# Kernel tuning notes

Measured on AMD Instinct MI355X. Metric: run time of the kernel, lower is better.

The kernel has to match this reference:

```python
import jax, jax.numpy as jnp
import numpy as np

NB, B, C, L = 4, 16, 256, 4096
BN_EPS = 1e-5


def setup_inputs() -> dict:
    key = jax.random.key(0)
    ks = jax.random.split(key, 10)
    s = 0.02
    return {
        "x": jax.random.normal(ks[0], (NB, B, C, L), jnp.float32),
        "Wq": jax.random.normal(ks[1], (NB, C, C), jnp.float32) * s,
        "bq": jax.random.normal(ks[2], (NB, C), jnp.float32) * s,
        "Wk": jax.random.normal(ks[3], (NB, C, C), jnp.float32) * s,
        "bk": jax.random.normal(ks[4], (NB, C), jnp.float32) * s,
        "Wv": jax.random.normal(ks[5], (NB, C, C), jnp.float32) * s,
        "bv": jax.random.normal(ks[6], (NB, C), jnp.float32) * s,
        "Wo": jax.random.normal(ks[7], (NB, C, C), jnp.float32) * s,
        "bo": jax.random.normal(ks[8], (NB, C), jnp.float32) * s,
        "gamma": jnp.ones((NB, C), jnp.float32),
        "beta": jnp.zeros((NB, C), jnp.float32),
        "edge_w": jnp.ones((NB, NB), jnp.float32),
        "branch_imp": jnp.ones((NB,), jnp.float32),
    }


def _proj(W, b, x):
    # 1x1 Conv1d == per-branch channel mixing: [nb,o,c] x [nb,B,c,L] -> [nb,B,o,L]
    return jnp.einsum('noc,nbcl->nbol', W, x) + b[:, None, :, None]


def reference(x, Wq, bq, Wk, bk, Wv, bv, Wo, bo, gamma, beta, edge_w, branch_imp):
    feat_dim = x.shape[2]
    scale = jnp.sqrt(jnp.asarray(feat_dim, x.dtype))
    q = _proj(Wq, bq, x)
    k = _proj(Wk, bk, x)
    v = _proj(Wv, bv, x)
    # descriptors: [nb, B, C, 2] = (mean over L, max over L)
    qd = jnp.stack([q.mean(axis=-1), q.max(axis=-1)], axis=-1)
    kd = jnp.stack([k.mean(axis=-1), k.max(axis=-1)], axis=-1)
    # mean over 2x2 bmm entries == (sum_p qd)(sum_q kd) summed over C, / 4
    scores = jnp.einsum('ibcp,jbcq->ijb', qd, kd) / (4.0 * scale)
    scores = scores * edge_w[:, :, None]
    attn = jax.nn.softmax(scores, axis=1) * jax.nn.softmax(branch_imp)[None, :, None]
    # weighted aggregation over source branches j
    agg = jnp.einsum('ijb,jbcl->ibcl', attn, v)
    out = _proj(Wo, bo, agg)
    # BatchNorm1d (training-mode batch statistics over B and L per channel, per branch)
    mean = out.mean(axis=(1, 3), keepdims=True)
    var = out.var(axis=(1, 3), keepdims=True)
    bn = (out - mean) * jax.lax.rsqrt(var + BN_EPS)
    bn = bn * gamma[:, None, :, None] + beta[:, None, :, None]
    return jax.nn.relu(bn) + x
```

## Files before the change

### kernel.cpp

```cpp
#include <hip/hip_runtime.h>
#include <stdint.h>
#include <stddef.h>

#define NBR 4
#define BSZ 16
#define CHN 256
#define LEN 4096
#define NB_B 64
#define BL   65536
#define BN_EPS 1e-5f
#define W_EL (NBR*CHN*CHN)

typedef unsigned short ushortT;
typedef unsigned short ushort4_t __attribute__((ext_vector_type(4)));
typedef unsigned short ushort8_t __attribute__((ext_vector_type(8)));
typedef short bf16x8 __attribute__((ext_vector_type(8)));
typedef float f32x4 __attribute__((ext_vector_type(4)));

__device__ __forceinline__ float bf2f(ushortT u) {
    return __uint_as_float(((unsigned)u) << 16);
}
__device__ __forceinline__ ushortT f2bf(float f) {
    unsigned b = __float_as_uint(f);
    return (ushortT)((b + 0x7FFFu + ((b >> 16) & 1u)) >> 16);
}
__device__ __forceinline__ unsigned encf(float f) {
    unsigned b = __float_as_uint(f);
    return (b & 0x80000000u) ? ~b : (b | 0x80000000u);
}
__device__ __forceinline__ float decf(unsigned u) {
    unsigned b = (u & 0x80000000u) ? (u ^ 0x80000000u) : ~u;
    return __uint_as_float(b);
}

__device__ __forceinline__ int swzX(int row, int cb) {
    return row * 512 + (cb ^ ((row & 7) << 4) ^ (((row >> 3) & 3) << 7));
}
__device__ __forceinline__ int swzW(int row, int cb) {
    return row * 128 + (cb ^ ((row & 7) << 4));
}

template <bool BF16IN>
__device__ __forceinline__ void stage_x(const void* act, ushortT* sX, int z, int lbase, int tid)
{
    const int ls = tid & 127;
    const int gh = tid >> 7;
    if (BF16IN) {
        const ushortT* xp = (const ushortT*)act + (size_t)z * CHN * LEN + lbase + ls;
#pragma unroll
        for (int g = 0; g < 16; ++g) {
            int c0 = (gh * 16 + g) * 8;
            ushort8_t u;
#pragma unroll
            for (int i = 0; i < 8; ++i) u[i] = xp[(size_t)(c0 + i) * LEN];
            *(ushort8_t*)((char*)sX + swzX(ls, c0 * 2)) = u;
        }
    } else {
        const float* xp = (const float*)act + (size_t)z * CHN * LEN + lbase + ls;
#pragma unroll
        for (int g = 0; g < 16; ++g) {
            int c0 = (gh * 16 + g) * 8;
            ushort8_t u;
#pragma unroll
            for (int i = 0; i < 8; ++i) u[i] = f2bf(xp[(size_t)(c0 + i) * LEN]);
            *(ushort8_t*)((char*)sX + swzX(ls, c0 * 2)) = u;
        }
    }
}

__device__ __forceinline__ void stage_w_load(const ushortT* Wb, int obase, int kb, int tid,
                                             ushort8_t wreg[4])
{
    const int r = tid >> 1;
    const int h = tid & 1;
    const ushortT* wp = Wb + (size_t)(obase + r) * CHN + kb + h * 32;
#pragma unroll
    for (int i = 0; i < 4; ++i) wreg[i] = *(const ushort8_t*)(wp + i * 8);
}
__device__ __forceinline__ void stage_w_write(ushortT* sW, int tid, const ushort8_t wreg[4])
{
    const int r = tid >> 1;
    const int h = tid & 1;
#pragma unroll
    for (int i = 0; i < 4; ++i)
        *(ushort8_t*)((char*)sW + swzW(r, h * 64 + i * 16)) = wreg[i];
}

__device__ __forceinline__ void mfma_chunk(const ushortT* sX, const ushortT* sW,
                                           f32x4 acc[4][4], int wr, int wc, int lane, int kb)
{
    const int am = wr * 64 + (lane & 15);
    const int bo = wc * 64 + (lane & 15);
    const int kg = (lane >> 4) * 16;
#pragma unroll
    for (int s = 0; s < 2; ++s) {
        bf16x8 a[4], b[4];
#pragma unroll
        for (int mf = 0; mf < 4; ++mf)
            a[mf] = *(const bf16x8*)((const char*)sX + swzX(am + mf * 16, kb * 2 + s * 64 + kg));
#pragma unroll
        for (int nf = 0; nf < 4; ++nf)
            b[nf] = *(const bf16x8*)((const char*)sW + swzW(bo + nf * 16, s * 64 + kg));
#pragma unroll
        for (int mf = 0; mf < 4; ++mf)
#pragma unroll
            for (int nf = 0; nf < 4; ++nf)
                acc[mf][nf] = __builtin_amdgcn_mfma_f32_16x16x32_bf16(a[mf], b[nf], acc[mf][nf], 0, 0, 0);
    }
}

__global__ __launch_bounds__(256, 2)
void qkv_kernel(const float* __restrict__ x, const ushortT* __restrict__ Wbf,
                const float* __restrict__ bv,
                float* __restrict__ qsum, unsigned* __restrict__ qmax,
                float* __restrict__ ksum, unsigned* __restrict__ kmax,
                ushortT* __restrict__ vbuf)
{
    __shared__ ushortT sX[128 * 256];
    __shared__ ushortT sW[128 * 64];
    const int tid = threadIdx.x;
    const int lane = tid & 63;
    const int wv = tid >> 6;
    const int wr = wv >> 1, wc = wv & 1;
    const int lbase = blockIdx.x * 128;
    const int z = blockIdx.y;
    const int n = z >> 4;

    stage_x<false>(x, sX, z, lbase, tid);

    ushort8_t wreg[4];
    stage_w_load(Wbf + (size_t)n * CHN * CHN, 0, 0, tid, wreg);

    for (int w = 0; w < 3; ++w) {
        for (int ot = 0; ot < 2; ++ot) {
            const int obase = ot * 128;
            f32x4 acc[4][4];
            const f32x4 z4 = {0.f, 0.f, 0.f, 0.f};
#pragma unroll
            for (int mf = 0; mf < 4; ++mf)
#pragma unroll
                for (int nf = 0; nf < 4; ++nf) acc[mf][nf] = z4;

#pragma unroll
            for (int kb = 0; kb < 4; ++kb) {
                __syncthreads();
                stage_w_write(sW, tid, wreg);
                int cidx = (w * 2 + ot) * 4 + kb + 1;
                if (cidx < 24) {
                    int nw = cidx >> 3, not_ = (cidx >> 2) & 1, nkb = cidx & 3;
                    stage_w_load(Wbf + ((size_t)nw * NBR + n) * CHN * CHN,
                                 not_ * 128, nkb * 64, tid, wreg);
                }
                __syncthreads();
                mfma_chunk(sX, sW, acc, wr, wc, lane, kb * 64);
            }

            if (w < 2) {
                float* rs = (w == 0) ? qsum : ksum;
                unsigned* rm = (w == 0) ? qmax : kmax;
#pragma unroll
                for (int nf = 0; nf < 4; ++nf) {
                    float s = 0.f, m = -3.4e38f;
#pragma unroll
                    for (int mf = 0; mf < 4; ++mf)
#pragma unroll
                        for (int r = 0; r < 4; ++r) {
                            float v = acc[mf][nf][r];
                            s += v; m = fmaxf(m, v);
                        }
                    s += __shfl_xor(s, 16); s += __shfl_xor(s, 32);
                    m = fmaxf(m, __shfl_xor(m, 16)); m = fmaxf(m, __shfl_xor(m, 32));
                    if (lane < 16) {
                        int o = obase + wc * 64 + nf * 16 + lane;
                        atomicAdd(&rs[z * CHN + o], s);
                        atomicMax(&rm[z * CHN + o], encf(m));
                    }
                }
            } else {
#pragma unroll
                for (int nf = 0; nf < 4; ++nf) {
                    int o = obase + wc * 64 + nf * 16 + (lane & 15);
                    float bvv = bv[n * CHN + o];
#pragma unroll
                    for (int mf = 0; mf < 4; ++mf) {
                        int l = lbase + wr * 64 + mf * 16 + ((lane >> 4) << 2);
                        ushort4_t u;
#pragma unroll
                        for (int r = 0; r < 4; ++r) u[r] = f2bf(acc[mf][nf][r] + bvv);
                        *(ushort4_t*)(vbuf + (size_t)(z * CHN + o) * LEN + l) = u;
                    }
                }
            }
        }
    }
}

__global__ __launch_bounds__(256, 2)
void ogemm_kernel(const ushortT* __restrict__ agg, const ushortT* __restrict__ Wbo,
                  const float* __restrict__ bo_,
                  float* __restrict__ bnsum, float* __restrict__ bnss,
                  ushortT* __restrict__ outpre)
{
    __shared__ ushortT sX[128 * 256];
    __shared__ ushortT sW[128 * 64];
    const int tid = threadIdx.x;
    const int lane = tid & 63;
    const int wv = tid >> 6;
    const int wr = wv >> 1, wc = wv & 1;
    const int lbase = blockIdx.x * 128;
    const int z = blockIdx.y;
    const int n = z >> 4;
    const ushortT* Wb = Wbo + (size_t)n * CHN * CHN;

    stage_x<true>(agg, sX, z, lbase, tid);

    ushort8_t wreg[4];
    stage_w_load(Wb, 0, 0, tid, wreg);

    for (int ot = 0; ot < 2; ++ot) {
        const int obase = ot * 128;
        f32x4 acc[4][4];
        const f32x4 z4 = {0.f, 0.f, 0.f, 0.f};
#pragma unroll
        for (int mf = 0; mf < 4; ++mf)
#pragma unroll
            for (int nf = 0; nf < 4; ++nf) acc[mf][nf] = z4;

#pragma unroll
        for (int kb = 0; kb < 4; ++kb) {
            __syncthreads();
            stage_w_write(sW, tid, wreg);
            int cidx = ot * 4 + kb + 1;
            if (cidx < 8) {
                int not_ = (cidx >> 2) & 1, nkb = cidx & 3;
                stage_w_load(Wb, not_ * 128, nkb * 64, tid, wreg);
            }
            __syncthreads();
            mfma_chunk(sX, sW, acc, wr, wc, lane, kb * 64);
        }

#pragma unroll
        for (int nf = 0; nf < 4; ++nf) {
            int o = obase + wc * 64 + nf * 16 + (lane & 15);
            float bb = bo_[n * CHN + o];
            float s = 0.f, q2 = 0.f;
#pragma unroll
            for (int mf = 0; mf < 4; ++mf) {
                int l = lbase + wr * 64 + mf * 16 + ((lane >> 4) << 2);
                ushort4_t u;
#pragma unroll
                for (int r = 0; r < 4; ++r) {
                    float v = acc[mf][nf][r] + bb;
                    u[r] = f2bf(v);
                    s += v; q2 += v * v;
                }
                *(ushort4_t*)(outpre + (size_t)(z * CHN + o) * LEN + l) = u;
            }
            s += __shfl_xor(s, 16); s += __shfl_xor(s, 32);
            q2 += __shfl_xor(q2, 16); q2 += __shfl_xor(q2, 32);
            if (lane < 16) {
                atomicAdd(&bnsum[n * CHN + o], s);
                atomicAdd(&bnss[n * CHN + o], q2);
            }
        }
    }
}

__global__ void wcvt_kernel(const float* __restrict__ Wq, const float* __restrict__ Wk,
                            const float* __restrict__ Wv, const float* __restrict__ Wo,
                            ushortT* __restrict__ Wbf)
{
    int t = blockIdx.x * 256 + threadIdx.x;
    const int per = W_EL / 4;
    if (t < 4 * per) {
        const float* srcs[4] = {Wq, Wk, Wv, Wo};
        int w = t / per;
        int r = t - w * per;
        float4 f = *(const float4*)(srcs[w] + (size_t)r * 4);
        ushort4_t u = {f2bf(f.x), f2bf(f.y), f2bf(f.z), f2bf(f.w)};
        *(ushort4_t*)(Wbf + (size_t)w * W_EL + (size_t)r * 4) = u;
    }
}

__global__ void attn_kernel(const float* __restrict__ qsum, const unsigned* __restrict__ qmax,
                            const float* __restrict__ ksum, const unsigned* __restrict__ kmax,
                            const float* __restrict__ bq, const float* __restrict__ bk,
                            const float* __restrict__ edge, const float* __restrict__ bimp,
                            float* __restrict__ attn)
{
    __shared__ float sc[NBR][NBR][BSZ];
    int tid = threadIdx.x;
    int i = tid >> 6, j = (tid >> 4) & 3, b = tid & 15;
    float s = 0.f;
    const float invL = 1.0f / (float)LEN;
    for (int c = 0; c < CHN; ++c) {
        int qi = (i * BSZ + b) * CHN + c;
        int ki = (j * BSZ + b) * CHN + c;
        float sq = qsum[qi] * invL + decf(qmax[qi]) + 2.f * bq[i * CHN + c];
        float sk = ksum[ki] * invL + decf(kmax[ki]) + 2.f * bk[j * CHN + c];
        s += sq * sk;
    }
    sc[i][j][b] = s * edge[i * 4 + j] * (1.0f / 64.0f);
    __syncthreads();
    if (tid < 64) {
        int ii = tid >> 4, bb = tid & 15;
        float m = -3.4e38f;
        for (int jj = 0; jj < 4; ++jj) m = fmaxf(m, sc[ii][jj][bb]);
        float e[4]; float sum = 0.f;
        for (int jj = 0; jj < 4; ++jj) { e[jj] = __expf(sc[ii][jj][bb] - m); sum += e[jj]; }
        float bm = fmaxf(fmaxf(bimp[0], bimp[1]), fmaxf(bimp[2], bimp[3]));
        float be[4]; float bs = 0.f;
        for (int jj = 0; jj < 4; ++jj) { be[jj] = __expf(bimp[jj] - bm); bs += be[jj]; }
        for (int jj = 0; jj < 4; ++jj)
            attn[(ii * 4 + jj) * BSZ + bb] = (e[jj] / sum) * (be[jj] / bs);
    }
}

__global__ __launch_bounds__(256)
void agg_kernel(const ushortT* __restrict__ v, const float* __restrict__ attn,
                ushortT* __restrict__ agg)
{
    __shared__ float sa[256];
    sa[threadIdx.x] = attn[threadIdx.x];
    __syncthreads();
    const long long U = (long long)BSZ * CHN * (LEN / 8);
    for (long long u = (long long)blockIdx.x * blockDim.x + threadIdx.x; u < U;
         u += (long long)gridDim.x * blockDim.x) {
        int l0 = (int)(u & 511) * 8;
        int c  = (int)(u >> 9) & 255;
        int b  = (int)(u >> 17);
        float vv[4][8];
#pragma unroll
        for (int j = 0; j < 4; ++j) {
            ushort8_t raw = *(const ushort8_t*)(v + (((size_t)(j * BSZ + b) * CHN + c) * LEN) + l0);
#pragma unroll
            for (int e = 0; e < 8; ++e) vv[j][e] = bf2f(raw[e]);
        }
#pragma unroll
        for (int i = 0; i < 4; ++i) {
            float a0 = sa[(i * 4 + 0) * BSZ + b];
            float a1 = sa[(i * 4 + 1) * BSZ + b];
            float a2 = sa[(i * 4 + 2) * BSZ + b];
            float a3 = sa[(i * 4 + 3) * BSZ + b];
            ushort8_t out;
#pragma unroll
            for (int e = 0; e < 8; ++e) {
                float r = a0 * vv[0][e] + a1 * vv[1][e] + a2 * vv[2][e] + a3 * vv[3][e];
                out[e] = f2bf(r);
            }
            *(ushort8_t*)(agg + (((size_t)(i * BSZ + b) * CHN + c) * LEN) + l0) = out;
        }
    }
}

__global__ void bnfin_kernel(const float* __restrict__ bnsum, const float* __restrict__ bnss,
                             const float* __restrict__ gamma, const float* __restrict__ beta,
                             float* __restrict__ scl, float* __restrict__ shf)
{
    int t = blockIdx.x * blockDim.x + threadIdx.x;
    if (t < NBR * CHN) {
        const float inv = 1.0f / (float)BL;
        float mean = bnsum[t] * inv;
        float var = bnss[t] * inv - mean * mean;
        float rs = rsqrtf(var + BN_EPS);
        float s = gamma[t] * rs;
        scl[t] = s;
        shf[t] = beta[t] - mean * s;
    }
}

__global__ __launch_bounds__(256)
void final_kernel(const ushortT* __restrict__ outpre, const float* __restrict__ x,
                  const float* __restrict__ scl, const float* __restrict__ shf,
                  float* __restrict__ out)
{
    const long long U = (long long)NB_B * CHN * (LEN / 8);
    for (long long u = (long long)blockIdx.x * blockDim.x + threadIdx.x; u < U;
         u += (long long)gridDim.x * blockDim.x) {
        int l0 = (int)(u & 511) * 8;
        int c  = (int)(u >> 9) & 255;
        int zz = (int)(u >> 17);
        int n  = zz >> 4;
        size_t base = ((size_t)zz * CHN + c) * LEN + l0;
        ushort8_t op = *(const ushort8_t*)(outpre + base);
        float4 x0 = *(const float4*)(x + base);
        float4 x1 = *(const float4*)(x + base + 4);
        float sc = scl[n * CHN + c];
        float sh = shf[n * CHN + c];
        float xr[8] = {x0.x, x0.y, x0.z, x0.w, x1.x, x1.y, x1.z, x1.w};
        float res[8];
#pragma unroll
        for (int e = 0; e < 8; ++e) {
            float bn = bf2f(op[e]) * sc + sh;
            res[e] = fmaxf(bn, 0.f) + xr[e];
        }
        float4 o0 = {res[0], res[1], res[2], res[3]};
        float4 o1 = {res[4], res[5], res[6], res[7]};
        *(float4*)(out + base) = o0;
        *(float4*)(out + base + 4) = o1;
    }
}

extern "C" void kernel_launch(void* const* d_in, const int* in_sizes, int n_in,
                              void* d_out, int out_size, void* d_ws, size_t ws_size,
                              hipStream_t stream)
{
    const float* x     = (const float*)d_in[0];
    const float* Wq    = (const float*)d_in[1];
    const float* bq    = (const float*)d_in[2];
    const float* Wk    = (const float*)d_in[3];
    const float* bk    = (const float*)d_in[4];
    const float* Wv    = (const float*)d_in[5];
    const float* bv    = (const float*)d_in[6];
    const float* Wo    = (const float*)d_in[7];
    const float* bo    = (const float*)d_in[8];
    const float* gamma = (const float*)d_in[9];
    const float* beta  = (const float*)d_in[10];
    const float* edge  = (const float*)d_in[11];
    const float* bimp  = (const float*)d_in[12];

    char* ws = (char*)d_ws;
    const size_t V_BYTES = (size_t)NBR * BSZ * CHN * LEN * 2;
    ushortT* vbuf = (ushortT*)ws;
    size_t off = V_BYTES;
    float*    qsum = (float*)(ws + off);    off += 65536;
    unsigned* qmax = (unsigned*)(ws + off); off += 65536;
    float*    ksum = (float*)(ws + off);    off += 65536;
    unsigned* kmax = (unsigned*)(ws + off); off += 65536;
    float*    attn = (float*)(ws + off);    off += 1024;
    float*    bnsum= (float*)(ws + off);    off += 4096;
    float*    bnss = (float*)(ws + off);    off += 4096;
    float*    scl  = (float*)(ws + off);    off += 4096;
    float*    shf  = (float*)(ws + off);    off += 4096;

    hipMemsetAsync(ws + V_BYTES, 0, off - V_BYTES, stream);

    ushortT* aggbuf = (ushortT*)d_out;
    float*   outf   = (float*)d_out;
    ushortT* Wbf = (ushortT*)((char*)d_out + ((size_t)134217728));

    wcvt_kernel<<<(4 * W_EL / 4 + 255) / 256, 256, 0, stream>>>(Wq, Wk, Wv, Wo, Wbf);

    dim3 gq(LEN / 128, NB_B);
    qkv_kernel<<<gq, 256, 0, stream>>>(x, Wbf, bv, qsum, qmax, ksum, kmax, vbuf);
    attn_kernel<<<1, 256, 0, stream>>>(qsum, qmax, ksum, kmax, bq, bk, edge, bimp, attn);
    agg_kernel<<<2048, 256, 0, stream>>>(vbuf, attn, aggbuf);
    ogemm_kernel<<<gq, 256, 0, stream>>>(aggbuf, Wbf + (size_t)3 * W_EL, bo, bnsum, bnss, vbuf);
    bnfin_kernel<<<4, 256, 0, stream>>>(bnsum, bnss, gamma, beta, scl, shf);
    final_kernel<<<8192, 256, 0, stream>>>(vbuf, x, scl, shf, outf);
}
```

Measured before the change: 524.9 us.

## Fuse attention aggregation into output GEMM staging and store V transposed

Removes the standalone aggregation kernel. The output-projection GEMM now builds its bf16 input tile itself by taking the attention-weighted sum of the four source-branch V tiles. To make that staging load contiguous, the QKV kernel writes V in an [L][C] transposed layout by swapping the MFMA operands for the V projection. The x staging in the QKV kernel is also reworked to do coalesced float4 loads through a shared-memory transpose buffer. The goal is to avoid the extra full read and write of the aggregated tensor, at the cost of each ogemm block reading four V tiles and more synchronisation during x staging.

```diff
diff --git a/kernel.cpp b/kernel.cpp
--- a/kernel.cpp
+++ b/kernel.cpp
@@ -40,34 +40,6 @@
     return row * 128 + (cb ^ ((row & 7) << 4));
 }
 
-template <bool BF16IN>
-__device__ __forceinline__ void stage_x(const void* act, ushortT* sX, int z, int lbase, int tid)
-{
-    const int ls = tid & 127;
-    const int gh = tid >> 7;
-    if (BF16IN) {
-        const ushortT* xp = (const ushortT*)act + (size_t)z * CHN * LEN + lbase + ls;
-#pragma unroll
-        for (int g = 0; g < 16; ++g) {
-            int c0 = (gh * 16 + g) * 8;
-            ushort8_t u;
-#pragma unroll
-            for (int i = 0; i < 8; ++i) u[i] = xp[(size_t)(c0 + i) * LEN];
-            *(ushort8_t*)((char*)sX + swzX(ls, c0 * 2)) = u;
-        }
-    } else {
-        const float* xp = (const float*)act + (size_t)z * CHN * LEN + lbase + ls;
-#pragma unroll
-        for (int g = 0; g < 16; ++g) {
-            int c0 = (gh * 16 + g) * 8;
-            ushort8_t u;
-#pragma unroll
-            for (int i = 0; i < 8; ++i) u[i] = f2bf(xp[(size_t)(c0 + i) * LEN]);
-            *(ushort8_t*)((char*)sX + swzX(ls, c0 * 2)) = u;
-        }
-    }
-}
-
 __device__ __forceinline__ void stage_w_load(const ushortT* Wb, int obase, int kb, int tid,
                                              ushort8_t wreg[4])
 {
@@ -86,6 +58,7 @@
         *(ushort8_t*)((char*)sW + swzW(r, h * 64 + i * 16)) = wreg[i];
 }
 
+template <bool SWAP>
 __device__ __forceinline__ void mfma_chunk(const ushortT* sX, const ushortT* sW,
                                            f32x4 acc[4][4], int wr, int wc, int lane, int kb)
 {
@@ -104,8 +77,12 @@
 #pragma unroll
         for (int mf = 0; mf < 4; ++mf)
 #pragma unroll
-            for (int nf = 0; nf < 4; ++nf)
-                acc[mf][nf] = __builtin_amdgcn_mfma_f32_16x16x32_bf16(a[mf], b[nf], acc[mf][nf], 0, 0, 0);
+            for (int nf = 0; nf < 4; ++nf) {
+                if (!SWAP)
+                    acc[mf][nf] = __builtin_amdgcn_mfma_f32_16x16x32_bf16(a[mf], b[nf], acc[mf][nf], 0, 0, 0);
+                else
+                    acc[nf][mf] = __builtin_amdgcn_mfma_f32_16x16x32_bf16(b[nf], a[mf], acc[nf][mf], 0, 0, 0);
+            }
     }
 }
 
@@ -114,7 +91,7 @@
                 const float* __restrict__ bv,
                 float* __restrict__ qsum, unsigned* __restrict__ qmax,
                 float* __restrict__ ksum, unsigned* __restrict__ kmax,
-                ushortT* __restrict__ vbuf)
+                ushortT* __restrict__ vT)
 {
     __shared__ ushortT sX[128 * 256];
     __shared__ ushortT sW[128 * 64];
@@ -126,10 +103,41 @@
     const int z = blockIdx.y;
     const int n = z >> 4;
 
-    stage_x<false>(x, sX, z, lbase, tid);
-
     ushort8_t wreg[4];
     stage_w_load(Wbf + (size_t)n * CHN * CHN, 0, 0, tid, wreg);
+
+    {
+        float* raw = (float*)sW;
+        const int tq = tid >> 5;
+        const int tl = tid & 31;
+        const int l  = tid & 127;
+        const int h  = tid >> 7;
+        const float* xz = x + (size_t)z * CHN * LEN + lbase;
+        float4 v4[4];
+#pragma unroll
+        for (int q = 0; q < 4; ++q)
+            v4[q] = *(const float4*)(xz + (size_t)(q * 8 + tq) * LEN + tl * 4);
+        for (int cc = 0; cc < 8; ++cc) {
+            __syncthreads();
+#pragma unroll
+            for (int q = 0; q < 4; ++q)
+                *(float4*)(raw + (q * 8 + tq) * 128 + tl * 4) = v4[q];
+            if (cc < 7) {
+#pragma unroll
+                for (int q = 0; q < 4; ++q)
+                    v4[q] = *(const float4*)(xz + (size_t)((cc + 1) * 32 + q * 8 + tq) * LEN + tl * 4);
+            }
+            __syncthreads();
+#pragma unroll
+            for (int p = 0; p < 2; ++p) {
+                int oct = h * 2 + p;
+                ushort8_t u8;
+#pragma unroll
+                for (int i = 0; i < 8; ++i) u8[i] = f2bf(raw[(oct * 8 + i) * 128 + l]);
+                *(ushort8_t*)((char*)sX + swzX(l, (cc * 32 + oct * 8) * 2)) = u8;
+            }
+        }
+    }
 
     for (int w = 0; w < 3; ++w) {
         for (int ot = 0; ot < 2; ++ot) {
@@ -152,7 +160,8 @@
                                  not_ * 128, nkb * 64, tid, wreg);
                 }
                 __syncthreads();
-                mfma_chunk(sX, sW, acc, wr, wc, lane, kb * 64);
+                if (w < 2) mfma_chunk<false>(sX, sW, acc, wr, wc, lane, kb * 64);
+                else       mfma_chunk<true >(sX, sW, acc, wr, wc, lane, kb * 64);
             }
 
             if (w < 2) {
@@ -179,15 +188,17 @@
             } else {
 #pragma unroll
                 for (int nf = 0; nf < 4; ++nf) {
-                    int o = obase + wc * 64 + nf * 16 + (lane & 15);
-                    float bvv = bv[n * CHN + o];
+                    int o0 = obase + wc * 64 + nf * 16 + ((lane >> 4) << 2);
+                    float b4[4];
+#pragma unroll
+                    for (int r = 0; r < 4; ++r) b4[r] = bv[n * CHN + o0 + r];
 #pragma unroll
                     for (int mf = 0; mf < 4; ++mf) {
-                        int l = lbase + wr * 64 + mf * 16 + ((lane >> 4) << 2);
+                        int l = lbase + wr * 64 + mf * 16 + (lane & 15);
                         ushort4_t u;
 #pragma unroll
-                        for (int r = 0; r < 4; ++r) u[r] = f2bf(acc[mf][nf][r] + bvv);
-                        *(ushort4_t*)(vbuf + (size_t)(z * CHN + o) * LEN + l) = u;
+                        for (int r = 0; r < 4; ++r) u[r] = f2bf(acc[nf][mf][r] + b4[r]);
+                        *(ushort4_t*)(vT + ((size_t)z * LEN + l) * CHN + o0) = u;
                     }
                 }
             }
@@ -196,8 +207,8 @@
 }
 
 __global__ __launch_bounds__(256, 2)
-void ogemm_kernel(const ushortT* __restrict__ agg, const ushortT* __restrict__ Wbo,
-                  const float* __restrict__ bo_,
+void ogemm_kernel(const ushortT* __restrict__ vT, const ushortT* __restrict__ Wbo,
+                  const float* __restrict__ attn, const float* __restrict__ bo_,
                   float* __restrict__ bnsum, float* __restrict__ bnss,
                   ushortT* __restrict__ outpre)
 {
@@ -210,12 +221,36 @@
     const int lbase = blockIdx.x * 128;
     const int z = blockIdx.y;
     const int n = z >> 4;
+    const int b_ = z & 15;
     const ushortT* Wb = Wbo + (size_t)n * CHN * CHN;
-
-    stage_x<true>(agg, sX, z, lbase, tid);
 
     ushort8_t wreg[4];
     stage_w_load(Wb, 0, 0, tid, wreg);
+
+    float aj[4];
+#pragma unroll
+    for (int j = 0; j < 4; ++j) aj[j] = attn[(n * 4 + j) * BSZ + b_];
+
+#pragma unroll 4
+    for (int u = 0; u < 16; ++u) {
+        int g = u * 256 + tid;
+        int l = g >> 5;
+        int cg = g & 31;
+        size_t boff = ((size_t)lbase + l) * CHN + cg * 8;
+        float acc8[8];
+#pragma unroll
+        for (int e = 0; e < 8; ++e) acc8[e] = 0.f;
+#pragma unroll
+        for (int j = 0; j < 4; ++j) {
+            ushort8_t r8 = *(const ushort8_t*)(vT + (size_t)(j * BSZ + b_) * LEN * CHN + boff);
+#pragma unroll
+            for (int e = 0; e < 8; ++e) acc8[e] += aj[j] * bf2f(r8[e]);
+        }
+        ushort8_t o8;
+#pragma unroll
+        for (int e = 0; e < 8; ++e) o8[e] = f2bf(acc8[e]);
+        *(ushort8_t*)((char*)sX + swzX(l, cg * 16)) = o8;
+    }
 
     for (int ot = 0; ot < 2; ++ot) {
         const int obase = ot * 128;
@@ -236,7 +271,7 @@
                 stage_w_load(Wb, not_ * 128, nkb * 64, tid, wreg);
             }
             __syncthreads();
-            mfma_chunk(sX, sW, acc, wr, wc, lane, kb * 64);
+            mfma_chunk<false>(sX, sW, acc, wr, wc, lane, kb * 64);
         }
 
 #pragma unroll
@@ -313,43 +348,6 @@
         for (int jj = 0; jj < 4; ++jj) { be[jj] = __expf(bimp[jj] - bm); bs += be[jj]; }
         for (int jj = 0; jj < 4; ++jj)
             attn[(ii * 4 + jj) * BSZ + bb] = (e[jj] / sum) * (be[jj] / bs);
-    }
-}
-
-__global__ __launch_bounds__(256)
-void agg_kernel(const ushortT* __restrict__ v, const float* __restrict__ attn,
-                ushortT* __restrict__ agg)
-{
-    __shared__ float sa[256];
-    sa[threadIdx.x] = attn[threadIdx.x];
-    __syncthreads();
-    const long long U = (long long)BSZ * CHN * (LEN / 8);
-    for (long long u = (long long)blockIdx.x * blockDim.x + threadIdx.x; u < U;
-         u += (long long)gridDim.x * blockDim.x) {
-        int l0 = (int)(u & 511) * 8;
-        int c  = (int)(u >> 9) & 255;
-        int b  = (int)(u >> 17);
-        float vv[4][8];
-#pragma unroll
-        for (int j = 0; j < 4; ++j) {
-            ushort8_t raw = *(const ushort8_t*)(v + (((size_t)(j * BSZ + b) * CHN + c) * LEN) + l0);
-#pragma unroll
-            for (int e = 0; e < 8; ++e) vv[j][e] = bf2f(raw[e]);
-        }
-#pragma unroll
-        for (int i = 0; i < 4; ++i) {
-            float a0 = sa[(i * 4 + 0) * BSZ + b];
-            float a1 = sa[(i * 4 + 1) * BSZ + b];
-            float a2 = sa[(i * 4 + 2) * BSZ + b];
-            float a3 = sa[(i * 4 + 3) * BSZ + b];
-            ushort8_t out;
-#pragma unroll
-            for (int e = 0; e < 8; ++e) {
-                float r = a0 * vv[0][e] + a1 * vv[1][e] + a2 * vv[2][e] + a3 * vv[3][e];
-                out[e] = f2bf(r);
-            }
-            *(ushort8_t*)(agg + (((size_t)(i * BSZ + b) * CHN + c) * LEN) + l0) = out;
-        }
     }
 }
 
@@ -420,9 +418,9 @@
     const float* bimp  = (const float*)d_in[12];
 
     char* ws = (char*)d_ws;
-    const size_t V_BYTES = (size_t)NBR * BSZ * CHN * LEN * 2;
-    ushortT* vbuf = (ushortT*)ws;
-    size_t off = V_BYTES;
+    const size_t P_BYTES = (size_t)NBR * BSZ * CHN * LEN * 2;
+    ushortT* outpre = (ushortT*)ws;
+    size_t off = P_BYTES;
     float*    qsum = (float*)(ws + off);    off += 65536;
     unsigned* qmax = (unsigned*)(ws + off); off += 65536;
     float*    ksum = (float*)(ws + off);    off += 65536;
@@ -433,19 +431,18 @@
     float*    scl  = (float*)(ws + off);    off += 4096;
     float*    shf  = (float*)(ws + off);    off += 4096;
 
-    hipMemsetAsync(ws + V_BYTES, 0, off - V_BYTES, stream);
-
-    ushortT* aggbuf = (ushortT*)d_out;
-    float*   outf   = (float*)d_out;
+    hipMemsetAsync(ws + P_BYTES, 0, off - P_BYTES, stream);
+
+    ushortT* vT  = (ushortT*)d_out;
     ushortT* Wbf = (ushortT*)((char*)d_out + ((size_t)134217728));
+    float*   outf = (float*)d_out;
 
     wcvt_kernel<<<(4 * W_EL / 4 + 255) / 256, 256, 0, stream>>>(Wq, Wk, Wv, Wo, Wbf);
 
     dim3 gq(LEN / 128, NB_B);
-    qkv_kernel<<<gq, 256, 0, stream>>>(x, Wbf, bv, qsum, qmax, ksum, kmax, vbuf);
+    qkv_kernel<<<gq, 256, 0, stream>>>(x, Wbf, bv, qsum, qmax, ksum, kmax, vT);
     attn_kernel<<<1, 256, 0, stream>>>(qsum, qmax, ksum, kmax, bq, bk, edge, bimp, attn);
-    agg_kernel<<<2048, 256, 0, stream>>>(vbuf, attn, aggbuf);
-    ogemm_kernel<<<gq, 256, 0, stream>>>(aggbuf, Wbf + (size_t)3 * W_EL, bo, bnsum, bnss, vbuf);
+    ogemm_kernel<<<gq, 256, 0, stream>>>(vT, Wbf + (size_t)3 * W_EL, attn, bo, bnsum, bnss, outpre);
     bnfin_kernel<<<4, 256, 0, stream>>>(bnsum, bnss, gamma, beta, scl, shf);
-    final_kernel<<<8192, 256, 0, stream>>>(vbuf, x, scl, shf, outf);
-}
+    final_kernel<<<8192, 256, 0, stream>>>(outpre, x, scl, shf, outf);
+}
```

After: 540.4 us. 1.03x slower.
